# Kernel tuning notes

Measured on AMD Instinct MI355X. Metric: run time of the kernel, lower is better.

## Reference

```python
import jax, jax.numpy as jnp
import numpy as np

HIDDEN = 1024
NUM_HEADS = 16
DK = 64  # key_and_query_dim
DV = 64  # value_dim
NEG_INF = -1.0e9


def setup_inputs() -> dict:
    key = jax.random.key(0)
    ks = jax.random.split(key, 12)
    B, S = 4, 2048
    scale = 0.02
    return {
        "q_hidden_inputs": jax.random.normal(ks[0], (B, S, HIDDEN), dtype=jnp.float32),
        "k_hidden_inputs": jax.random.normal(ks[1], (B, S, HIDDEN), dtype=jnp.float32),
        "v_hidden_inputs": jax.random.normal(ks[2], (B, S, HIDDEN), dtype=jnp.float32),
        "mask": jax.random.randint(ks[3], (B, S, S), 0, 2) > 0,
        # per-head projection weights, stacked over heads: [H, hidden, dk/dv]
        "wq": jax.random.normal(ks[4], (NUM_HEADS, HIDDEN, DK), dtype=jnp.float32) * scale,
        "bq": jax.random.normal(ks[5], (NUM_HEADS, DK), dtype=jnp.float32) * scale,
        "wk": jax.random.normal(ks[6], (NUM_HEADS, HIDDEN, DK), dtype=jnp.float32) * scale,
        "bk": jax.random.normal(ks[7], (NUM_HEADS, DK), dtype=jnp.float32) * scale,
        "wv": jax.random.normal(ks[8], (NUM_HEADS, HIDDEN, DV), dtype=jnp.float32) * scale,
        "bv": jax.random.normal(ks[9], (NUM_HEADS, DV), dtype=jnp.float32) * scale,
        # output projection: [H*dv, hidden]
        "wo": jax.random.normal(ks[10], (NUM_HEADS * DV, HIDDEN), dtype=jnp.float32) * scale,
        "bo": jax.random.normal(ks[11], (HIDDEN,), dtype=jnp.float32) * scale,
    }


def reference(q_hidden_inputs, k_hidden_inputs, v_hidden_inputs, mask,
              wq, bq, wk, bk, wv, bv, wo, bo):
    # Per-head linear projections, vectorized over heads: [B, H, S, dk]
    q = jnp.einsum('bsd,hdk->bhsk', q_hidden_inputs, wq) + bq[None, :, None, :]
    k = jnp.einsum('bsd,hdk->bhsk', k_hidden_inputs, wk) + bk[None, :, None, :]
    v = jnp.einsum('bsd,hdv->bhsv', v_hidden_inputs, wv) + bv[None, :, None, :]
    # scores: [B, H, Sq, Sk]
    scores = jnp.einsum('bhsk,bhtk->bhst', q, k) / jnp.sqrt(jnp.float32(DK))
    scores = jnp.where(mask[:, None, :, :], scores, NEG_INF)
    attn = jax.nn.softmax(scores, axis=-1)
    out = jnp.einsum('bhst,bhtv->bhsv', attn, v)  # [B, H, Sq, dv]
    B, H, Sq, Dv = out.shape
    # heads concatenated along last dim in head order (same as torch.cat)
    out = jnp.transpose(out, (0, 2, 1, 3)).reshape(B, Sq, H * Dv)
    return out @ wo + bo
```

## Files before the change

### kernel.cpp

```cpp
#include <hip/hip_runtime.h>
#include <stdint.h>


typedef __bf16 bf16x8_t __attribute__((ext_vector_type(8)));
typedef float f32x4_t __attribute__((ext_vector_type(4)));
typedef short s16x4_t __attribute__((ext_vector_type(4)));

#define HID   1024
#define SLEN  2048
#define BATCH 4
#define NH    16
#define MROWS 8192
#define L2E   1.44269504f

__device__ __forceinline__ unsigned short bfbits(float f) {
  union { __bf16 h; unsigned short u; } v; v.h = (__bf16)f; return v.u;
}
__device__ __forceinline__ unsigned int packbf(float a, float b) {
  return (unsigned int)bfbits(a) | ((unsigned int)bfbits(b) << 16);
}
__device__ __forceinline__ float fast_exp2(float x) {
#if __has_builtin(__builtin_amdgcn_exp2f)
  return __builtin_amdgcn_exp2f(x);
#else
  return __exp2f(x);
#endif
}

__device__ __forceinline__ f32x4_t mfma16x16(s16x4_t a, s16x4_t b, f32x4_t c) {
#if __has_builtin(__builtin_amdgcn_mfma_f32_16x16x16bf16_1k)
  return __builtin_amdgcn_mfma_f32_16x16x16bf16_1k(a, b, c, 0, 0, 0);
#else
  asm("v_mfma_f32_16x16x16_bf16 %0, %1, %2, %0" : "+v"(c) : "v"(a), "v"(b));
  return c;
#endif
}

__device__ __forceinline__ void gload_lds16(const void* g, void* l) {
  __builtin_amdgcn_global_load_lds((const __attribute__((address_space(1))) void*)g,
                                   (__attribute__((address_space(3))) void*)l,
                                   16, 0, 0);
}

__device__ __forceinline__ bf16x8_t frag_ld(const unsigned short* lds, int row, int sblk) {
  int sp = sblk ^ (row & 7);
  return *(const bf16x8_t*)(lds + (row << 6) + (sp << 3));
}

__global__ void detect_mask_kernel(const unsigned int* __restrict__ m,
                                   unsigned int* __restrict__ flag) {
  unsigned int v = m[threadIdx.x];
  unsigned long long b = __ballot(v > 1u);
  if (threadIdx.x == 0) flag[0] = 0u;
  __syncthreads();
  if ((threadIdx.x & 63) == 0 && b) atomicOr(flag, 1u);
}

__global__ __launch_bounds__(256) void mask_bits_kernel(const void* __restrict__ maskp,
    const unsigned int* __restrict__ flag, unsigned long long* __restrict__ bits) {
  int lane = threadIdx.x & 63, wv = threadIdx.x >> 6;
  bool bytemask = flag[0] != 0u;
  size_t w0 = (size_t)blockIdx.x * 64 + (size_t)wv * 16;
  for (int it = 0; it < 16; ++it) {
    size_t word = w0 + it;
    unsigned int v;
    if (bytemask) v = ((const unsigned char*)maskp)[word * 64 + lane];
    else          v = ((const unsigned int*)maskp)[word * 64 + lane];
    unsigned long long bm = __ballot(v != 0u);
    if (lane == 0) bits[word] = bm;
  }
}

__global__ __launch_bounds__(256) void cvt_x_kernel(const float* __restrict__ src,
                                                    unsigned short* __restrict__ xb) {
  size_t base = (size_t)blockIdx.x * 1024 + (size_t)threadIdx.x * 4;
  float4 v = *(const float4*)(src + base);
  ushort4 o;
  o.x = bfbits(v.x); o.y = bfbits(v.y); o.z = bfbits(v.z); o.w = bfbits(v.w);
  *(ushort4*)(xb + base) = o;
}

__global__ __launch_bounds__(256) void pack_w_kernel(const float* __restrict__ wq,
    const float* __restrict__ wk, const float* __restrict__ wv,
    const float* __restrict__ wo, unsigned short* __restrict__ wt) {
  int z = blockIdx.y;
  int id = blockIdx.x * 256 + threadIdx.x;
  int n = id >> 8;
  int d0 = (id & 255) << 2;
  ushort4 o;
  if (z < 3) {
    const float* w = z == 0 ? wq : (z == 1 ? wk : wv);
    const float* base = w + (size_t)(n >> 6) * (HID * 64) + (n & 63);
    o.x = bfbits(base[(size_t)(d0 + 0) * 64]);
    o.y = bfbits(base[(size_t)(d0 + 1) * 64]);
    o.z = bfbits(base[(size_t)(d0 + 2) * 64]);
    o.w = bfbits(base[(size_t)(d0 + 3) * 64]);
  } else {
    o.x = bfbits(wo[(size_t)(d0 + 0) * HID + n]);
    o.y = bfbits(wo[(size_t)(d0 + 1) * HID + n]);
    o.z = bfbits(wo[(size_t)(d0 + 2) * HID + n]);
    o.w = bfbits(wo[(size_t)(d0 + 3) * HID + n]);
  }
  *(ushort4*)(wt + (size_t)z * (HID * HID) + (size_t)n * HID + d0) = o;
}

__global__ __launch_bounds__(256) void transpose_v_kernel(
    const unsigned short* __restrict__ V, unsigned short* __restrict__ VT) {
  __shared__ unsigned int t[64 * 32];
  int tid = threadIdx.x;
  int bh = blockIdx.y;
  int s0 = blockIdx.x * 64;
  const unsigned short* Vb = V + (size_t)bh * (SLEN * 64);
  int sp = tid >> 3, d0 = (tid & 7) << 3;
  const unsigned short* vs = Vb + (size_t)(s0 + sp * 2) * 64 + d0;
  bf16x8_t v0 = *(const bf16x8_t*)(vs);
  bf16x8_t v1 = *(const bf16x8_t*)(vs + 64);
  union { __bf16 b[8]; unsigned short u[8]; } a0, a1;
  *(bf16x8_t*)a0.b = v0; *(bf16x8_t*)a1.b = v1;
#pragma unroll
  for (int e = 0; e < 8; ++e) {
    int d = d0 + e;
    unsigned int val = (unsigned int)a0.u[e] | ((unsigned int)a1.u[e] << 16);
    int slot = (sp >> 2) ^ (d & 7);
    t[d * 32 + slot * 4 + (sp & 3)] = val;
  }
  __syncthreads();
#pragma unroll
  for (int it = 0; it < 2; ++it) {
    int gid = it * 256 + tid;
    int d = gid >> 3, slot = gid & 7;
    uint4 vv = *(const uint4*)(t + d * 32 + ((slot ^ (d & 7)) << 2));
    *(uint4*)(VT + (size_t)bh * (64 * SLEN) + (size_t)d * SLEN + s0 + slot * 8) = vv;
  }
}

__device__ __forceinline__ void gemm_stage(const unsigned short* __restrict__ A,
    const unsigned short* __restrict__ B, unsigned short* la, unsigned short* lb,
    int tid, int w, int kt) {
#pragma unroll
  for (int i = 0; i < 4; ++i) {
    int flat = i * 256 + tid;
    int row = flat >> 3;
    int sl = (flat & 7) ^ (row & 7);
    gload_lds16(A + (size_t)row * HID + kt + sl * 8, la + ((i * 256 + w * 64) << 3));
    gload_lds16(B + (size_t)row * HID + kt + sl * 8, lb + ((i * 256 + w * 64) << 3));
  }
}

__device__ __forceinline__ void gemm_tile_mainloop(const unsigned short* __restrict__ A,
    const unsigned short* __restrict__ B, unsigned short (*lA)[128 * 64],
    unsigned short (*lB)[128 * 64], int tid, f32x4_t (&acc)[4][4]) {
  int lane = tid & 63, w = tid >> 6;
  int wr = (w >> 1) << 6, wc = (w & 1) << 6;
  gemm_stage(A, B, lA[0], lB[0], tid, w, 0);
  __syncthreads();
  int cur = 0;
  for (int kt = 0; kt < HID; kt += 64) {
    if (kt + 64 < HID)
      gemm_stage(A, B, lA[cur ^ 1], lB[cur ^ 1], tid, w, kt + 64);
    const unsigned short* la = lA[cur];
    const unsigned short* lb = lB[cur];
#pragma unroll
    for (int kk = 0; kk < 2; ++kk) {
      bf16x8_t af[4], bfr[4];
#pragma unroll
      for (int mi = 0; mi < 4; ++mi)
        af[mi] = frag_ld(la, wr + mi * 16 + (lane & 15), kk * 4 + (lane >> 4));
#pragma unroll
      for (int ni = 0; ni < 4; ++ni)
        bfr[ni] = frag_ld(lb, wc + ni * 16 + (lane & 15), kk * 4 + (lane >> 4));
#pragma unroll
      for (int mi = 0; mi < 4; ++mi)
#pragma unroll
        for (int ni = 0; ni < 4; ++ni)
          acc[mi][ni] = __builtin_amdgcn_mfma_f32_16x16x32_bf16(af[mi], bfr[ni],
                                                                acc[mi][ni], 0, 0, 0);
    }
    __syncthreads();
    cur ^= 1;
  }
}

__global__ __launch_bounds__(256) void gemm_qkv_kernel(
    const unsigned short* __restrict__ Ain, const unsigned short* __restrict__ Bin,
    const float* __restrict__ bias, unsigned short* __restrict__ Out, float scale) {
  __shared__ __align__(16) unsigned short lA[2][128 * 64];
  __shared__ __align__(16) unsigned short lB[2][128 * 64];
  int m0 = blockIdx.x * 128, n0 = blockIdx.y * 128;
  const unsigned short* A = Ain + (size_t)m0 * HID;
  const unsigned short* B = Bin + (size_t)n0 * HID;
  f32x4_t acc[4][4] = {};
  int tid = threadIdx.x;
  gemm_tile_mainloop(A, B, lA, lB, tid, acc);
  int lane = tid & 63, w = tid >> 6;
  int wr = (w >> 1) << 6, wc = (w & 1) << 6;
#pragma unroll
  for (int mi = 0; mi < 4; ++mi)
#pragma unroll
    for (int ni = 0; ni < 4; ++ni) {
      int col = n0 + wc + ni * 16 + (lane & 15);
      float bb = bias[col];
      int h = col >> 6, d = col & 63;
#pragma unroll
      for (int r = 0; r < 4; ++r) {
        int row = m0 + wr + mi * 16 + ((lane >> 4) << 2) + r;
        int b = row >> 11, s = row & 2047;
        Out[((((size_t)b * NH + h) * SLEN + s) << 6) + d] = bfbits((acc[mi][ni][r] + bb) * scale);
      }
    }
}

__global__ __launch_bounds__(256) void gemm_out_kernel(
    const unsigned short* __restrict__ Ob, const unsigned short* __restrict__ WoT,
    const float* __restrict__ bo, float* __restrict__ out) {
  __shared__ __align__(16) unsigned short lA[2][128 * 64];
  __shared__ __align__(16) unsigned short lB[2][128 * 64];
  int m0 = blockIdx.x * 128, n0 = blockIdx.y * 128;
  const unsigned short* A = Ob + (size_t)m0 * HID;
  const unsigned short* B = WoT + (size_t)n0 * HID;
  f32x4_t acc[4][4] = {};
  int tid = threadIdx.x;
  gemm_tile_mainloop(A, B, lA, lB, tid, acc);
  int lane = tid & 63, w = tid >> 6;
  int wr = (w >> 1) << 6, wc = (w & 1) << 6;
#pragma unroll
  for (int mi = 0; mi < 4; ++mi)
#pragma unroll
    for (int ni = 0; ni < 4; ++ni) {
      int col = n0 + wc + ni * 16 + (lane & 15);
      float bb = bo[col];
#pragma unroll
      for (int r = 0; r < 4; ++r) {
        int row = m0 + wr + mi * 16 + ((lane >> 4) << 2) + r;
        out[(size_t)row * HID + col] = acc[mi][ni][r] + bb;
      }
    }
}

__global__ __launch_bounds__(256) void attn_kernel(
    const unsigned short* __restrict__ Q, const unsigned short* __restrict__ K,
    const unsigned short* __restrict__ VT, const unsigned long long* __restrict__ mbits,
    unsigned short* __restrict__ O) {
  __shared__ __align__(16) unsigned short lK[2][64 * 64];
  __shared__ __align__(16) unsigned short lV[2][64 * 64];
  int tid = threadIdx.x, lane = tid & 63, w = tid >> 6;
  int g = lane >> 4, ql = lane & 15;
  int bid = blockIdx.x;
  int bh = (bid & 7) * 8 + ((bid >> 3) >> 4);
  int qt = (bid >> 3) & 15;
  int b = bh >> 4, h = bh & 15;
  int q0 = qt * 128;
  const unsigned short* Qb = Q + (size_t)bh * (SLEN * 64);

  int f0 = tid, f1 = 256 + tid;
  int r0 = f0 >> 3, r1 = f1 >> 3;
  int s0 = (f0 & 7) ^ (r0 & 7), s1 = (f1 & 7) ^ (r1 & 7);
  const unsigned short* kS0 = K + (size_t)bh * (SLEN * 64) + (size_t)r0 * 64 + s0 * 8;
  const unsigned short* kS1 = K + (size_t)bh * (SLEN * 64) + (size_t)r1 * 64 + s1 * 8;
  const unsigned short* vS0 = VT + (size_t)bh * (64 * SLEN) + (size_t)r0 * SLEN + s0 * 8;
  const unsigned short* vS1 = VT + (size_t)bh * (64 * SLEN) + (size_t)r1 * SLEN + s1 * 8;
  int d0off = (0 * 256 + w * 64) << 3;
  int d1off = (1 * 256 + w * 64) << 3;
  const unsigned long long* mp0 = mbits + ((size_t)b * SLEN + (q0 + w * 32 + ql)) * 32;
  const unsigned long long* mp1 = mp0 + 16 * 32;

  int vbyte0 = (ql << 7) + (((g >> 1) ^ (ql & 7)) << 4) + ((g & 1) << 3);

  bf16x8_t qf[2][2];
#pragma unroll
  for (int mi = 0; mi < 2; ++mi)
#pragma unroll
    for (int kk = 0; kk < 2; ++kk) {
      int row = q0 + w * 32 + mi * 16 + ql;
      qf[mi][kk] = *(const bf16x8_t*)(Qb + (size_t)row * 64 + kk * 32 + g * 8);
    }

  s16x4_t ones4 = {0x3F80, 0x3F80, 0x3F80, 0x3F80};

  f32x4_t aco[2][4] = {};
  f32x4_t slacc[2] = {};

  gload_lds16(kS0, (unsigned short*)lK[0] + d0off);
  gload_lds16(kS1, (unsigned short*)lK[0] + d1off);
  gload_lds16(vS0, (unsigned short*)lV[0] + d0off);
  gload_lds16(vS1, (unsigned short*)lV[0] + d1off);
  kS0 += 4096; kS1 += 4096; vS0 += 64; vS1 += 64;
  __syncthreads();

  int cur = 0;
  for (int kt = 0; kt < SLEN / 64; ++kt) {
    if (kt + 1 < SLEN / 64) {
      unsigned short* kn = (unsigned short*)lK[cur ^ 1];
      unsigned short* vn = (unsigned short*)lV[cur ^ 1];
      gload_lds16(kS0, kn + d0off);
      gload_lds16(kS1, kn + d1off);
      gload_lds16(vS0, vn + d0off);
      gload_lds16(vS1, vn + d1off);
      kS0 += 4096; kS1 += 4096; vS0 += 64; vS1 += 64;
    }

    unsigned long long bg0 = mp0[kt] >> (4 * g);
    unsigned long long bg1 = mp1[kt] >> (4 * g);

    const unsigned short* kbuf = lK[cur];
    const unsigned short* vbuf = lV[cur];
    f32x4_t st[2][4];
#pragma unroll
    for (int mi = 0; mi < 2; ++mi)
#pragma unroll
      for (int ni = 0; ni < 4; ++ni) st[mi][ni] = (f32x4_t){0.f, 0.f, 0.f, 0.f};
    __builtin_amdgcn_s_setprio(1);
#pragma unroll
    for (int kk = 0; kk < 2; ++kk) {
      bf16x8_t kf[4];
#pragma unroll
      for (int ni = 0; ni < 4; ++ni)
        kf[ni] = frag_ld(kbuf, ni * 16 + ql, kk * 4 + g);
#pragma unroll
      for (int mi = 0; mi < 2; ++mi)
#pragma unroll
        for (int ni = 0; ni < 4; ++ni)
          st[mi][ni] = __builtin_amdgcn_mfma_f32_16x16x32_bf16(kf[ni], qf[mi][kk],
                                                               st[mi][ni], 0, 0, 0);
    }
    __builtin_amdgcn_s_setprio(0);

    unsigned int pb[2][4][2];
#pragma unroll
    for (int mi = 0; mi < 2; ++mi) {
      unsigned long long bgs = mi ? bg1 : bg0;
      unsigned int mw0 = (unsigned int)bgs;
      unsigned int mw1 = (unsigned int)(bgs >> 32);
#pragma unroll
      for (int ni = 0; ni < 4; ++ni) {
        unsigned int mword = (ni < 2) ? mw0 : mw1;
        int base = (ni & 1) * 16;
        float p[4];
#pragma unroll
        for (int r = 0; r < 4; ++r) {
          float e = fast_exp2(st[mi][ni][r]);
          p[r] = ((mword >> (base + r)) & 1u) ? e : 0.f;
        }
        pb[mi][ni][0] = packbf(p[0], p[1]);
        pb[mi][ni][1] = packbf(p[2], p[3]);
      }
    }

    __builtin_amdgcn_s_setprio(1);
#pragma unroll
    for (int c = 0; c < 4; ++c) {
      s16x4_t vfa[4];
#pragma unroll
      for (int dvf = 0; dvf < 4; ++dvf) {
        union { uint2 u; s16x4_t s; } t;
        t.u = *(const uint2*)((const char*)vbuf + ((vbyte0 ^ (c << 5)) + dvf * 2048));
        vfa[dvf] = t.s;
      }
#pragma unroll
      for (int mi = 0; mi < 2; ++mi) {
        union { unsigned int u[2]; s16x4_t s; } pp;
        pp.u[0] = pb[mi][c][0]; pp.u[1] = pb[mi][c][1];
        slacc[mi] = mfma16x16(ones4, pp.s, slacc[mi]);
#pragma unroll
        for (int dvf = 0; dvf < 4; ++dvf)
          aco[mi][dvf] = mfma16x16(vfa[dvf], pp.s, aco[mi][dvf]);
      }
    }
    __builtin_amdgcn_s_setprio(0);

    __syncthreads();
    cur ^= 1;
  }

  unsigned short* eb = (unsigned short*)lK;
#pragma unroll
  for (int mi = 0; mi < 2; ++mi) {
    float inv = 1.0f / slacc[mi][0];
    int prow = w * 32 + mi * 16 + ql;
#pragma unroll
    for (int dvf = 0; dvf < 4; ++dvf) {
      unsigned int lo = packbf(aco[mi][dvf][0] * inv, aco[mi][dvf][1] * inv);
      unsigned int hi = packbf(aco[mi][dvf][2] * inv, aco[mi][dvf][3] * inv);
      int sl = (2 * dvf + (g >> 1)) ^ (prow & 7);
      *(uint2*)((char*)eb + prow * 128 + sl * 16 + (g & 1) * 8) = make_uint2(lo, hi);
    }
  }
#pragma unroll
  for (int it = 0; it < 8; ++it) {
    int rloc = g + 4 * it;
    int row = w * 32 + rloc;
    int sl = (ql >> 1) ^ (row & 7);
    uint2 v = *(const uint2*)((const char*)eb + row * 128 + sl * 16 + (ql & 1) * 8);
    int qrow = q0 + row;
    *(uint2*)(O + (((size_t)b * SLEN + qrow) << 10) + h * 64 + ql * 4) = v;
  }
}

extern "C" void kernel_launch(void* const* d_in, const int* in_sizes, int n_in,
                              void* d_out, int out_size, void* d_ws, size_t ws_size,
                              hipStream_t stream) {
  (void)in_sizes; (void)n_in; (void)out_size; (void)ws_size;
  const float* xq = (const float*)d_in[0];
  const float* xk = (const float*)d_in[1];
  const float* xv = (const float*)d_in[2];
  const void*  mask = d_in[3];
  const float* wq = (const float*)d_in[4];
  const float* bq = (const float*)d_in[5];
  const float* wk = (const float*)d_in[6];
  const float* bk = (const float*)d_in[7];
  const float* wv = (const float*)d_in[8];
  const float* bv = (const float*)d_in[9];
  const float* wo = (const float*)d_in[10];
  const float* bo = (const float*)d_in[11];
  float* out = (float*)d_out;

  char* ws = (char*)d_ws;
  unsigned short* XbZ  = (unsigned short*)(ws);
  unsigned short* Ob   = (unsigned short*)(ws);
  unsigned short* Wt   = (unsigned short*)(ws + 16777216ull);
  unsigned short* QKV  = (unsigned short*)(ws + 25165824ull);
  unsigned int*   flag = (unsigned int*)(ws + 75497472ull);
  unsigned long long* mbits = (unsigned long long*)d_out;
  unsigned short* VTp = (unsigned short*)((char*)d_out + 2097152ull);

  const float* xs[3]   = {xq, xk, xv};
  const float* bias[3] = {bq, bk, bv};

  detect_mask_kernel<<<1, 256, 0, stream>>>((const unsigned int*)mask, flag);
  mask_bits_kernel<<<4096, 256, 0, stream>>>(mask, flag, mbits);
  pack_w_kernel<<<dim3(1024, 4), 256, 0, stream>>>(wq, wk, wv, wo, Wt);
  for (int z = 0; z < 3; ++z) {
    cvt_x_kernel<<<8192, 256, 0, stream>>>(xs[z], XbZ);
    gemm_qkv_kernel<<<dim3(64, 8), 256, 0, stream>>>(
        XbZ, Wt + (size_t)z * (HID * HID), bias[z],
        QKV + (size_t)z * ((size_t)MROWS * 1024), z == 0 ? 0.125f * L2E : 1.0f);
  }
  transpose_v_kernel<<<dim3(32, 64), 256, 0, stream>>>(QKV + 16777216ull, VTp);
  attn_kernel<<<1024, 256, 0, stream>>>(QKV, QKV + 8388608ull, VTp, mbits, Ob);
  gemm_out_kernel<<<dim3(64, 8), 256, 0, stream>>>(Ob, Wt + 3ull * (HID * HID), bo, out);
}
```

Baseline: 300.6 us.

## Switch attention kernel to 32x32x16 MFMA with permlane-swapped P fragments

Rewrites the attention inner loop to use 32x32x16 bf16 MFMA for both QK^T and PV instead of 16x16 tiles, which changes the fragment layouts for Q, K, V and P. The P fragments are rearranged with v_permlane32_swap so they can feed the PV MFMA directly. The row-sum is now computed with scalar adds plus one cross-half shuffle rather than an extra MFMA against a ones vector. The aim is fewer MFMA and LDS fragment instructions per tile. The trade-offs are higher register pressure from the 16-wide accumulators and the 32-element p array, plus reliance on gfx950-specific instructions.

```diff
diff --git a/kernel.cpp b/kernel.cpp
--- a/kernel.cpp
+++ b/kernel.cpp
@@ -4,7 +4,7 @@
 
 typedef __bf16 bf16x8_t __attribute__((ext_vector_type(8)));
 typedef float f32x4_t __attribute__((ext_vector_type(4)));
-typedef short s16x4_t __attribute__((ext_vector_type(4)));
+typedef float f32x16_t __attribute__((ext_vector_type(16)));
 
 #define HID   1024
 #define SLEN  2048
@@ -24,15 +24,6 @@
   return __builtin_amdgcn_exp2f(x);
 #else
   return __exp2f(x);
-#endif
-}
-
-__device__ __forceinline__ f32x4_t mfma16x16(s16x4_t a, s16x4_t b, f32x4_t c) {
-#if __has_builtin(__builtin_amdgcn_mfma_f32_16x16x16bf16_1k)
-  return __builtin_amdgcn_mfma_f32_16x16x16bf16_1k(a, b, c, 0, 0, 0);
-#else
-  asm("v_mfma_f32_16x16x16_bf16 %0, %1, %2, %0" : "+v"(c) : "v"(a), "v"(b));
-  return c;
 #endif
 }
 
@@ -244,12 +235,13 @@
   __shared__ __align__(16) unsigned short lK[2][64 * 64];
   __shared__ __align__(16) unsigned short lV[2][64 * 64];
   int tid = threadIdx.x, lane = tid & 63, w = tid >> 6;
-  int g = lane >> 4, ql = lane & 15;
+  int h32 = lane >> 5, l31 = lane & 31;
   int bid = blockIdx.x;
   int bh = (bid & 7) * 8 + ((bid >> 3) >> 4);
   int qt = (bid >> 3) & 15;
   int b = bh >> 4, h = bh & 15;
   int q0 = qt * 128;
+  int q = q0 + w * 32 + l31;
   const unsigned short* Qb = Q + (size_t)bh * (SLEN * 64);
 
   int f0 = tid, f1 = 256 + tid;
@@ -261,24 +253,15 @@
   const unsigned short* vS1 = VT + (size_t)bh * (64 * SLEN) + (size_t)r1 * SLEN + s1 * 8;
   int d0off = (0 * 256 + w * 64) << 3;
   int d1off = (1 * 256 + w * 64) << 3;
-  const unsigned long long* mp0 = mbits + ((size_t)b * SLEN + (q0 + w * 32 + ql)) * 32;
-  const unsigned long long* mp1 = mp0 + 16 * 32;
-
-  int vbyte0 = (ql << 7) + (((g >> 1) ^ (ql & 7)) << 4) + ((g & 1) << 3);
-
-  bf16x8_t qf[2][2];
-#pragma unroll
-  for (int mi = 0; mi < 2; ++mi)
-#pragma unroll
-    for (int kk = 0; kk < 2; ++kk) {
-      int row = q0 + w * 32 + mi * 16 + ql;
-      qf[mi][kk] = *(const bf16x8_t*)(Qb + (size_t)row * 64 + kk * 32 + g * 8);
-    }
-
-  s16x4_t ones4 = {0x3F80, 0x3F80, 0x3F80, 0x3F80};
-
-  f32x4_t aco[2][4] = {};
-  f32x4_t slacc[2] = {};
+  const unsigned long long* mp = mbits + ((size_t)b * SLEN + q) * 32;
+
+  bf16x8_t qf[4];
+#pragma unroll
+  for (int ks = 0; ks < 4; ++ks)
+    qf[ks] = *(const bf16x8_t*)(Qb + (size_t)q * 64 + ks * 16 + h32 * 8);
+
+  f32x16_t aco[2] = {};
+  float lsum = 0.f;
 
   gload_lds16(kS0, (unsigned short*)lK[0] + d0off);
   gload_lds16(kS1, (unsigned short*)lK[0] + d1off);
@@ -299,71 +282,63 @@
       kS0 += 4096; kS1 += 4096; vS0 += 64; vS1 += 64;
     }
 
-    unsigned long long bg0 = mp0[kt] >> (4 * g);
-    unsigned long long bg1 = mp1[kt] >> (4 * g);
+    unsigned long long bg = mp[kt];
+    unsigned int mwl = (unsigned int)(bg >> (4 * h32));
+    unsigned int mwh = (unsigned int)(bg >> (32 + 4 * h32));
 
     const unsigned short* kbuf = lK[cur];
     const unsigned short* vbuf = lV[cur];
-    f32x4_t st[2][4];
-#pragma unroll
-    for (int mi = 0; mi < 2; ++mi)
-#pragma unroll
-      for (int ni = 0; ni < 4; ++ni) st[mi][ni] = (f32x4_t){0.f, 0.f, 0.f, 0.f};
+
+    f32x16_t st[2] = {};
     __builtin_amdgcn_s_setprio(1);
 #pragma unroll
-    for (int kk = 0; kk < 2; ++kk) {
-      bf16x8_t kf[4];
-#pragma unroll
-      for (int ni = 0; ni < 4; ++ni)
-        kf[ni] = frag_ld(kbuf, ni * 16 + ql, kk * 4 + g);
-#pragma unroll
-      for (int mi = 0; mi < 2; ++mi)
-#pragma unroll
-        for (int ni = 0; ni < 4; ++ni)
-          st[mi][ni] = __builtin_amdgcn_mfma_f32_16x16x32_bf16(kf[ni], qf[mi][kk],
-                                                               st[mi][ni], 0, 0, 0);
+    for (int kvb = 0; kvb < 2; ++kvb) {
+#pragma unroll
+      for (int ks = 0; ks < 4; ++ks) {
+        int row = kvb * 32 + l31;
+        int slot = (2 * ks + h32) ^ (row & 7);
+        bf16x8_t kf = *(const bf16x8_t*)(kbuf + (row << 6) + (slot << 3));
+        st[kvb] = __builtin_amdgcn_mfma_f32_32x32x16_bf16(kf, qf[ks], st[kvb], 0, 0, 0);
+      }
     }
     __builtin_amdgcn_s_setprio(0);
 
-    unsigned int pb[2][4][2];
-#pragma unroll
-    for (int mi = 0; mi < 2; ++mi) {
-      unsigned long long bgs = mi ? bg1 : bg0;
-      unsigned int mw0 = (unsigned int)bgs;
-      unsigned int mw1 = (unsigned int)(bgs >> 32);
-#pragma unroll
-      for (int ni = 0; ni < 4; ++ni) {
-        unsigned int mword = (ni < 2) ? mw0 : mw1;
-        int base = (ni & 1) * 16;
-        float p[4];
-#pragma unroll
-        for (int r = 0; r < 4; ++r) {
-          float e = fast_exp2(st[mi][ni][r]);
-          p[r] = ((mword >> (base + r)) & 1u) ? e : 0.f;
-        }
-        pb[mi][ni][0] = packbf(p[0], p[1]);
-        pb[mi][ni][1] = packbf(p[2], p[3]);
-      }
-    }
+    float p[32];
+#pragma unroll
+    for (int kvb = 0; kvb < 2; ++kvb) {
+      unsigned int mw = kvb ? mwh : mwl;
+#pragma unroll
+      for (int i = 0; i < 16; ++i) {
+        float e = fast_exp2(st[kvb][i]);
+        int pos = (i & 3) + 8 * (i >> 2);
+        p[kvb * 16 + i] = ((mw >> pos) & 1u) ? e : 0.f;
+      }
+    }
+    float t8[8];
+#pragma unroll
+    for (int i = 0; i < 8; ++i)
+      t8[i] = (p[4 * i] + p[4 * i + 1]) + (p[4 * i + 2] + p[4 * i + 3]);
+    float sml = ((t8[0] + t8[1]) + (t8[2] + t8[3])) + ((t8[4] + t8[5]) + (t8[6] + t8[7]));
+    lsum += sml + __shfl_xor(sml, 32, 64);
+    unsigned int pw[16];
+#pragma unroll
+    for (int j = 0; j < 16; ++j) pw[j] = packbf(p[2 * j], p[2 * j + 1]);
 
     __builtin_amdgcn_s_setprio(1);
 #pragma unroll
-    for (int c = 0; c < 4; ++c) {
-      s16x4_t vfa[4];
-#pragma unroll
-      for (int dvf = 0; dvf < 4; ++dvf) {
-        union { uint2 u; s16x4_t s; } t;
-        t.u = *(const uint2*)((const char*)vbuf + ((vbyte0 ^ (c << 5)) + dvf * 2048));
-        vfa[dvf] = t.s;
-      }
-#pragma unroll
-      for (int mi = 0; mi < 2; ++mi) {
-        union { unsigned int u[2]; s16x4_t s; } pp;
-        pp.u[0] = pb[mi][c][0]; pp.u[1] = pb[mi][c][1];
-        slacc[mi] = mfma16x16(ones4, pp.s, slacc[mi]);
-#pragma unroll
-        for (int dvf = 0; dvf < 4; ++dvf)
-          aco[mi][dvf] = mfma16x16(vfa[dvf], pp.s, aco[mi][dvf]);
+    for (int s4 = 0; s4 < 4; ++s4) {
+      unsigned int c0 = pw[4 * s4 + 0], c1 = pw[4 * s4 + 1];
+      unsigned int c2 = pw[4 * s4 + 2], c3 = pw[4 * s4 + 3];
+      asm("v_permlane32_swap_b32 %0, %1" : "+v"(c0), "+v"(c2));
+      asm("v_permlane32_swap_b32 %0, %1" : "+v"(c1), "+v"(c3));
+      union { unsigned int u[4]; bf16x8_t v; } pf;
+      pf.u[0] = c0; pf.u[1] = c1; pf.u[2] = c2; pf.u[3] = c3;
+#pragma unroll
+      for (int dvb = 0; dvb < 2; ++dvb) {
+        int row = dvb * 32 + l31;
+        int slot = (2 * s4 + h32) ^ (row & 7);
+        bf16x8_t vf = *(const bf16x8_t*)(vbuf + (row << 6) + (slot << 3));
+        aco[dvb] = __builtin_amdgcn_mfma_f32_32x32x16_bf16(vf, pf.v, aco[dvb], 0, 0, 0);
       }
     }
     __builtin_amdgcn_s_setprio(0);
@@ -373,25 +348,29 @@
   }
 
   unsigned short* eb = (unsigned short*)lK;
-#pragma unroll
-  for (int mi = 0; mi < 2; ++mi) {
-    float inv = 1.0f / slacc[mi][0];
-    int prow = w * 32 + mi * 16 + ql;
-#pragma unroll
-    for (int dvf = 0; dvf < 4; ++dvf) {
-      unsigned int lo = packbf(aco[mi][dvf][0] * inv, aco[mi][dvf][1] * inv);
-      unsigned int hi = packbf(aco[mi][dvf][2] * inv, aco[mi][dvf][3] * inv);
-      int sl = (2 * dvf + (g >> 1)) ^ (prow & 7);
-      *(uint2*)((char*)eb + prow * 128 + sl * 16 + (g & 1) * 8) = make_uint2(lo, hi);
-    }
-  }
+  float inv = 1.0f / lsum;
+  int row = w * 32 + l31;
+#pragma unroll
+  for (int dvb = 0; dvb < 2; ++dvb)
+#pragma unroll
+    for (int i = 0; i < 4; ++i)
+#pragma unroll
+      for (int jj = 0; jj < 2; ++jj) {
+        float a0 = aco[dvb][4 * i + 2 * jj] * inv;
+        float a1 = aco[dvb][4 * i + 2 * jj + 1] * inv;
+        unsigned int v = packbf(a0, a1);
+        int dv0 = 32 * dvb + 8 * i + 4 * h32 + 2 * jj;
+        int slot = (dv0 >> 3) ^ (row & 7);
+        *(unsigned int*)((char*)eb + row * 128 + slot * 16 + (dv0 & 7) * 2) = v;
+      }
+  int g = lane >> 4, ql = lane & 15;
 #pragma unroll
   for (int it = 0; it < 8; ++it) {
     int rloc = g + 4 * it;
-    int row = w * 32 + rloc;
-    int sl = (ql >> 1) ^ (row & 7);
-    uint2 v = *(const uint2*)((const char*)eb + row * 128 + sl * 16 + (ql & 1) * 8);
-    int qrow = q0 + row;
+    int rrow = w * 32 + rloc;
+    int sl = (ql >> 1) ^ (rrow & 7);
+    uint2 v = *(const uint2*)((const char*)eb + rrow * 128 + sl * 16 + (ql & 1) * 8);
+    int qrow = q0 + rrow;
     *(uint2*)(O + (((size_t)b * SLEN + qrow) << 10) + h * 64 + ql * 4) = v;
   }
 }
```

Measured after the change: 302.2 us. No clear change (+0.5%).

## Batch Q/K/V conversion and projection GEMMs into single launches with K=32 tiles

Applied to the files above, without the earlier changes.

Converts all three hidden inputs to bf16 in one launch and runs the Q, K, V projection GEMMs as one 3D-grid kernel instead of three sequential cvt+GEMM pairs. The QKV GEMM now uses a 32-wide K tile with a new LDS swizzle, halving shared memory per block so more blocks can stay resident. Workspace is rearranged so Xk and Xv live in the output buffer, and the mask bitpacking moves after the GEMM. The intent is to fill the GPU with 1536 blocks at once and cut launch and tail overhead, at the cost of twice as many k-loop iterations and barriers in the QKV GEMM.

```diff
diff --git a/kernel.cpp b/kernel.cpp
--- a/kernel.cpp
+++ b/kernel.cpp
@@ -45,6 +45,10 @@
 __device__ __forceinline__ bf16x8_t frag_ld(const unsigned short* lds, int row, int sblk) {
   int sp = sblk ^ (row & 7);
   return *(const bf16x8_t*)(lds + (row << 6) + (sp << 3));
+}
+__device__ __forceinline__ bf16x8_t frag_ld32(const unsigned short* lds, int row, int g) {
+  int sp = g ^ (row & 3) ^ ((row >> 2) & 3);
+  return *(const bf16x8_t*)(lds + (row << 5) + (sp << 3));
 }
 
 __global__ void detect_mask_kernel(const unsigned int* __restrict__ m,
@@ -71,13 +75,18 @@
   }
 }
 
-__global__ __launch_bounds__(256) void cvt_x_kernel(const float* __restrict__ src,
-                                                    unsigned short* __restrict__ xb) {
+__global__ __launch_bounds__(256) void cvt_x_kernel(const float* __restrict__ xq,
+    const float* __restrict__ xk, const float* __restrict__ xv,
+    unsigned short* __restrict__ dq, unsigned short* __restrict__ dk,
+    unsigned short* __restrict__ dv) {
+  int z = blockIdx.y;
+  const float* src = z == 0 ? xq : (z == 1 ? xk : xv);
+  unsigned short* dst = z == 0 ? dq : (z == 1 ? dk : dv);
   size_t base = (size_t)blockIdx.x * 1024 + (size_t)threadIdx.x * 4;
   float4 v = *(const float4*)(src + base);
   ushort4 o;
   o.x = bfbits(v.x); o.y = bfbits(v.y); o.z = bfbits(v.z); o.w = bfbits(v.w);
-  *(ushort4*)(xb + base) = o;
+  *(ushort4*)(dst + base) = o;
 }
 
 __global__ __launch_bounds__(256) void pack_w_kernel(const float* __restrict__ wq,
@@ -134,6 +143,81 @@
   }
 }
 
+__device__ __forceinline__ void gemm_stage32(const unsigned short* __restrict__ A,
+    const unsigned short* __restrict__ B, unsigned short* la, unsigned short* lb,
+    int tid, int w, int kt) {
+#pragma unroll
+  for (int i = 0; i < 2; ++i) {
+    int flat = i * 256 + tid;
+    int row = flat >> 2;
+    int sl = (flat & 3) ^ (row & 3) ^ ((row >> 2) & 3);
+    gload_lds16(A + (size_t)row * HID + kt + sl * 8, la + ((i * 256 + w * 64) << 3));
+    gload_lds16(B + (size_t)row * HID + kt + sl * 8, lb + ((i * 256 + w * 64) << 3));
+  }
+}
+
+__global__ __launch_bounds__(256) void gemm_qkv_kernel(
+    const unsigned short* __restrict__ Xq, const unsigned short* __restrict__ Xk,
+    const unsigned short* __restrict__ Xv, const unsigned short* __restrict__ Wt,
+    const float* __restrict__ bq, const float* __restrict__ bk,
+    const float* __restrict__ bv, unsigned short* __restrict__ QKV) {
+  __shared__ __align__(16) unsigned short lA[2][128 * 32];
+  __shared__ __align__(16) unsigned short lB[2][128 * 32];
+  int z = blockIdx.z;
+  const unsigned short* Ain = z == 0 ? Xq : (z == 1 ? Xk : Xv);
+  const float* bias = z == 0 ? bq : (z == 1 ? bk : bv);
+  float scale = z == 0 ? 0.125f * L2E : 1.0f;
+  int m0 = blockIdx.x * 128, n0 = blockIdx.y * 128;
+  const unsigned short* A = Ain + (size_t)m0 * HID;
+  const unsigned short* B = Wt + (size_t)z * (HID * HID) + (size_t)n0 * HID;
+  unsigned short* Out = QKV + (size_t)z * ((size_t)MROWS * 1024);
+
+  f32x4_t acc[4][4] = {};
+  int tid = threadIdx.x, lane = tid & 63, w = tid >> 6;
+  int wr = (w >> 1) << 6, wc = (w & 1) << 6;
+  int ql = lane & 15, g = lane >> 4;
+
+  gemm_stage32(A, B, lA[0], lB[0], tid, w, 0);
+  __syncthreads();
+  int cur = 0;
+  for (int kt = 0; kt < HID; kt += 32) {
+    if (kt + 32 < HID)
+      gemm_stage32(A, B, lA[cur ^ 1], lB[cur ^ 1], tid, w, kt + 32);
+    const unsigned short* la = lA[cur];
+    const unsigned short* lb = lB[cur];
+    bf16x8_t af[4], bfr[4];
+#pragma unroll
+    for (int mi = 0; mi < 4; ++mi)
+      af[mi] = frag_ld32(la, wr + mi * 16 + ql, g);
+#pragma unroll
+    for (int ni = 0; ni < 4; ++ni)
+      bfr[ni] = frag_ld32(lb, wc + ni * 16 + ql, g);
+#pragma unroll
+    for (int mi = 0; mi < 4; ++mi)
+#pragma unroll
+      for (int ni = 0; ni < 4; ++ni)
+        acc[mi][ni] = __builtin_amdgcn_mfma_f32_16x16x32_bf16(af[mi], bfr[ni],
+                                                              acc[mi][ni], 0, 0, 0);
+    __syncthreads();
+    cur ^= 1;
+  }
+
+#pragma unroll
+  for (int mi = 0; mi < 4; ++mi)
+#pragma unroll
+    for (int ni = 0; ni < 4; ++ni) {
+      int col = n0 + wc + ni * 16 + ql;
+      float bb = bias[col];
+      int h = col >> 6, d = col & 63;
+#pragma unroll
+      for (int r = 0; r < 4; ++r) {
+        int row = m0 + wr + mi * 16 + (g << 2) + r;
+        int b = row >> 11, s = row & 2047;
+        Out[((((size_t)b * NH + h) * SLEN + s) << 6) + d] = bfbits((acc[mi][ni][r] + bb) * scale);
+      }
+    }
+}
+
 __device__ __forceinline__ void gemm_stage(const unsigned short* __restrict__ A,
     const unsigned short* __restrict__ B, unsigned short* la, unsigned short* lb,
     int tid, int w, int kt) {
@@ -147,9 +231,16 @@
   }
 }
 
-__device__ __forceinline__ void gemm_tile_mainloop(const unsigned short* __restrict__ A,
-    const unsigned short* __restrict__ B, unsigned short (*lA)[128 * 64],
-    unsigned short (*lB)[128 * 64], int tid, f32x4_t (&acc)[4][4]) {
+__global__ __launch_bounds__(256) void gemm_out_kernel(
+    const unsigned short* __restrict__ Ob, const unsigned short* __restrict__ WoT,
+    const float* __restrict__ bo, float* __restrict__ out) {
+  __shared__ __align__(16) unsigned short lA[2][128 * 64];
+  __shared__ __align__(16) unsigned short lB[2][128 * 64];
+  int m0 = blockIdx.x * 128, n0 = blockIdx.y * 128;
+  const unsigned short* A = Ob + (size_t)m0 * HID;
+  const unsigned short* B = WoT + (size_t)n0 * HID;
+  f32x4_t acc[4][4] = {};
+  int tid = threadIdx.x;
   int lane = tid & 63, w = tid >> 6;
   int wr = (w >> 1) << 6, wc = (w & 1) << 6;
   gemm_stage(A, B, lA[0], lB[0], tid, w, 0);
@@ -179,50 +270,6 @@
     __syncthreads();
     cur ^= 1;
   }
-}
-
-__global__ __launch_bounds__(256) void gemm_qkv_kernel(
-    const unsigned short* __restrict__ Ain, const unsigned short* __restrict__ Bin,
-    const float* __restrict__ bias, unsigned short* __restrict__ Out, float scale) {
-  __shared__ __align__(16) unsigned short lA[2][128 * 64];
-  __shared__ __align__(16) unsigned short lB[2][128 * 64];
-  int m0 = blockIdx.x * 128, n0 = blockIdx.y * 128;
-  const unsigned short* A = Ain + (size_t)m0 * HID;
-  const unsigned short* B = Bin + (size_t)n0 * HID;
-  f32x4_t acc[4][4] = {};
-  int tid = threadIdx.x;
-  gemm_tile_mainloop(A, B, lA, lB, tid, acc);
-  int lane = tid & 63, w = tid >> 6;
-  int wr = (w >> 1) << 6, wc = (w & 1) << 6;
-#pragma unroll
-  for (int mi = 0; mi < 4; ++mi)
-#pragma unroll
-    for (int ni = 0; ni < 4; ++ni) {
-      int col = n0 + wc + ni * 16 + (lane & 15);
-      float bb = bias[col];
-      int h = col >> 6, d = col & 63;
-#pragma unroll
-      for (int r = 0; r < 4; ++r) {
-        int row = m0 + wr + mi * 16 + ((lane >> 4) << 2) + r;
-        int b = row >> 11, s = row & 2047;
-        Out[((((size_t)b * NH + h) * SLEN + s) << 6) + d] = bfbits((acc[mi][ni][r] + bb) * scale);
-      }
-    }
-}
-
-__global__ __launch_bounds__(256) void gemm_out_kernel(
-    const unsigned short* __restrict__ Ob, const unsigned short* __restrict__ WoT,
-    const float* __restrict__ bo, float* __restrict__ out) {
-  __shared__ __align__(16) unsigned short lA[2][128 * 64];
-  __shared__ __align__(16) unsigned short lB[2][128 * 64];
-  int m0 = blockIdx.x * 128, n0 = blockIdx.y * 128;
-  const unsigned short* A = Ob + (size_t)m0 * HID;
-  const unsigned short* B = WoT + (size_t)n0 * HID;
-  f32x4_t acc[4][4] = {};
-  int tid = threadIdx.x;
-  gemm_tile_mainloop(A, B, lA, lB, tid, acc);
-  int lane = tid & 63, w = tid >> 6;
-  int wr = (w >> 1) << 6, wc = (w & 1) << 6;
 #pragma unroll
   for (int mi = 0; mi < 4; ++mi)
 #pragma unroll
@@ -415,26 +462,21 @@
   float* out = (float*)d_out;
 
   char* ws = (char*)d_ws;
-  unsigned short* XbZ  = (unsigned short*)(ws);
+  unsigned short* Xq   = (unsigned short*)(ws);
   unsigned short* Ob   = (unsigned short*)(ws);
   unsigned short* Wt   = (unsigned short*)(ws + 16777216ull);
   unsigned short* QKV  = (unsigned short*)(ws + 25165824ull);
   unsigned int*   flag = (unsigned int*)(ws + 75497472ull);
-  unsigned long long* mbits = (unsigned long long*)d_out;
-  unsigned short* VTp = (unsigned short*)((char*)d_out + 2097152ull);
-
-  const float* xs[3]   = {xq, xk, xv};
-  const float* bias[3] = {bq, bk, bv};
+  unsigned short* Xk  = (unsigned short*)d_out;
+  unsigned short* Xv  = (unsigned short*)((char*)d_out + 16777216ull);
+  unsigned short* VTp = (unsigned short*)d_out;
+  unsigned long long* mbits = (unsigned long long*)((char*)d_out + 16777216ull);
 
   detect_mask_kernel<<<1, 256, 0, stream>>>((const unsigned int*)mask, flag);
+  pack_w_kernel<<<dim3(1024, 4), 256, 0, stream>>>(wq, wk, wv, wo, Wt);
+  cvt_x_kernel<<<dim3(8192, 3), 256, 0, stream>>>(xq, xk, xv, Xq, Xk, Xv);
+  gemm_qkv_kernel<<<dim3(64, 8, 3), 256, 0, stream>>>(Xq, Xk, Xv, Wt, bq, bk, bv, QKV);
   mask_bits_kernel<<<4096, 256, 0, stream>>>(mask, flag, mbits);
-  pack_w_kernel<<<dim3(1024, 4), 256, 0, stream>>>(wq, wk, wv, wo, Wt);
-  for (int z = 0; z < 3; ++z) {
-    cvt_x_kernel<<<8192, 256, 0, stream>>>(xs[z], XbZ);
-    gemm_qkv_kernel<<<dim3(64, 8), 256, 0, stream>>>(
-        XbZ, Wt + (size_t)z * (HID * HID), bias[z],
-        QKV + (size_t)z * ((size_t)MROWS * 1024), z == 0 ? 0.125f * L2E : 1.0f);
-  }
   transpose_v_kernel<<<dim3(32, 64), 256, 0, stream>>>(QKV + 16777216ull, VTp);
   attn_kernel<<<1024, 256, 0, stream>>>(QKV, QKV + 8388608ull, VTp, mbits, Ob);
   gemm_out_kernel<<<dim3(64, 8), 256, 0, stream>>>(Ob, Wt + 3ull * (HID * HID), bo, out);
```

New measurement: 297.2 us. About the same (-1.1%).
